# Kernel optimization log

Measured on AMD Instinct MI355X. Metric: run time of the kernel, lower is better.

Reference implementation:

```python
import jax, jax.numpy as jnp
import numpy as np

B, C, H, W = 8, 384, 32, 32
KEYS, HEADS, U = 16, 4, 1
VS = C // HEADS
N = H * W
BN_EPS = 1e-5


def setup_inputs() -> dict:
    key = jax.random.key(0)
    ks = jax.random.split(key, 8)
    x = jax.random.normal(ks[0], (B, C, H, W), dtype=jnp.float32)
    # 1x1 convs (spectral-normalized in torch; SN only rescales the weight,
    # so a plain weight matrix computes the same functional form)
    Wq = jax.random.normal(ks[1], (KEYS * HEADS, C), dtype=jnp.float32) * 0.02
    Wk = jax.random.normal(ks[2], (KEYS * U, C), dtype=jnp.float32) * 0.02
    Wv = jax.random.normal(ks[3], (VS * U, C), dtype=jnp.float32) * 0.02
    # BatchNorm affine params (torch code xavier-inits weight, zeros bias)
    gamma_q = jax.random.normal(ks[4], (KEYS * HEADS,), dtype=jnp.float32)
    beta_q = jnp.zeros((KEYS * HEADS,), dtype=jnp.float32)
    gamma_v = jax.random.normal(ks[5], (VS * U,), dtype=jnp.float32)
    beta_v = jnp.zeros((VS * U,), dtype=jnp.float32)
    pos_emb = jax.random.normal(ks[6], (N, N, KEYS, U), dtype=jnp.float32)
    return {"x": x, "Wq": Wq, "Wk": Wk, "Wv": Wv,
            "gamma_q": gamma_q, "beta_q": beta_q,
            "gamma_v": gamma_v, "beta_v": beta_v,
            "pos_emb": pos_emb}


def _bn(z, gamma, beta):
    # z: (B, Ch, N); BatchNorm2d in training mode: biased batch stats over (B, N)
    mean = jnp.mean(z, axis=(0, 2), keepdims=True)
    var = jnp.var(z, axis=(0, 2), keepdims=True)
    zn = (z - mean) * jax.lax.rsqrt(var + BN_EPS)
    return zn * gamma[None, :, None] + beta[None, :, None]


def reference(x, Wq, Wk, Wv, gamma_q, beta_q, gamma_v, beta_v, pos_emb):
    xf = x.reshape(B, C, N)                       # 1x1 conv == per-pixel matmul
    q = jnp.einsum('oc,bcn->bon', Wq, xf)         # (B, KEYS*HEADS, N)
    k = jnp.einsum('oc,bcn->bon', Wk, xf)         # (B, KEYS*U, N)
    v = jnp.einsum('oc,bcn->bon', Wv, xf)         # (B, VS*U, N)
    q = _bn(q, gamma_q, beta_q)
    v = _bn(v, gamma_v, beta_v)
    q = q.reshape(B, HEADS, KEYS, N)
    k = k.reshape(B, U, KEYS, N)
    v = v.reshape(B, U, VS, N)
    k = jax.nn.softmax(k, axis=-1)
    lambdac = jnp.einsum('bukm,buvm->bkv', k, v)          # content lambda
    Yc = jnp.einsum('bhkn,bkv->bhvn', q, lambdac)
    lambdap = jnp.einsum('nmku,buvm->bnkv', pos_emb, v)   # position lambda (B,N,K,V)
    Yp = jnp.einsum('bhkn,bnkv->bhvn', q, lambdap)
    Y = (Yc + Yp).reshape(B, C, H, W)
    return Y
```

## Files before the change

### kernel.cpp

```cpp
#include <hip/hip_runtime.h>

typedef __attribute__((ext_vector_type(8))) short short8;
typedef __attribute__((ext_vector_type(16))) float floatx16;
typedef __attribute__((ext_vector_type(4))) float floatx4;
typedef unsigned short ushort16_t;
typedef unsigned int uint32;

#define BB 8
#define CC 384
#define NPIX 1024
#define TOTCH 176
#define BN_EPS 1e-5f

__device__ __forceinline__ ushort16_t f2bf(float x) {
    uint32 u = __float_as_uint(x);
    u += 0x7FFFu + ((u >> 16) & 1u);
    return (ushort16_t)(u >> 16);
}
__device__ __forceinline__ uint32 pk2(float a, float b) {
    uint32 ua = __float_as_uint(a); ua += 0x7FFFu + ((ua >> 16) & 1u);
    uint32 ub = __float_as_uint(b); ub += 0x7FFFu + ((ub >> 16) & 1u);
    return (ua >> 16) | (ub & 0xFFFF0000u);
}
__device__ __forceinline__ void dma16(const ushort16_t* g, ushort16_t* l) {
    __builtin_amdgcn_global_load_lds(
        (const __attribute__((address_space(1))) uint32*)g,
        (__attribute__((address_space(3))) uint32*)l, 16, 0, 0);
}
__device__ __forceinline__ int div48(int x) {
    return (int)(((unsigned)x * 21846u) >> 20);
}


__global__ __launch_bounds__(256) void k_xt(const float* __restrict__ x,
    const float* __restrict__ Wq, const float* __restrict__ Wk,
    const float* __restrict__ Wv,
    ushort16_t* __restrict__ xbf, ushort16_t* __restrict__ wbf)
{
    int bx = blockIdx.x, t = threadIdx.x;
    if (bx < 256) {
        __shared__ __align__(16) ushort16_t T[32 * 392];
        int col0 = bx * 32;
        int b = col0 >> 10, nbase = col0 & 1023;
        const float* xb = x + (size_t)b * (CC * NPIX) + nbase;
        #pragma unroll
        for (int j = 0; j < 12; ++j) {
            int idx = t + 256 * j;
            int c = idx >> 3, ng = idx & 7;
            float4 f = *(const float4*)(xb + (size_t)c * NPIX + ng * 4);
            int n = ng * 4;
            T[(n + 0) * 392 + c] = f2bf(f.x);
            T[(n + 1) * 392 + c] = f2bf(f.y);
            T[(n + 2) * 392 + c] = f2bf(f.z);
            T[(n + 3) * 392 + c] = f2bf(f.w);
        }
        __syncthreads();
        #pragma unroll
        for (int j = 0; j < 6; ++j) {
            int task = t + 256 * j;
            int col = div48(task);
            int ch  = task - col * 48;
            uint4 w = *(const uint4*)&T[col * 392 + ch * 8];
            *(uint4*)&xbf[(size_t)(col0 + col) * CC + ch * 8] = w;
        }
    } else {
        #pragma unroll
        for (int jj = 0; jj < 9; ++jj) {
            int idx8 = ((bx - 256) * 9 + jj) * 256 + t;
            int row = div48(idx8);
            int g   = idx8 - row * 48;
            float4 f0, f1;
            if (row < 176) {
                const float* src;
                if (row < 64)       src = Wq + (size_t)row * CC;
                else if (row < 80)  src = Wk + (size_t)(row - 64) * CC;
                else                src = Wv + (size_t)(row - 80) * CC;
                f0 = *(const float4*)(src + g * 8);
                f1 = *(const float4*)(src + g * 8 + 4);
            } else {
                f0.x = f0.y = f0.z = f0.w = 0.f;
                f1 = f0;
            }
            uint4 w;
            w.x = pk2(f0.x, f0.y); w.y = pk2(f0.z, f0.w);
            w.z = pk2(f1.x, f1.y); w.w = pk2(f1.z, f1.w);
            *(uint4*)&wbf[(size_t)row * CC + g * 8] = w;
        }
    }
}

__global__ __launch_bounds__(256) void k_proj(const ushort16_t* __restrict__ xbf,
    const ushort16_t* __restrict__ wbf, float* __restrict__ qkv)
{
    int t = threadIdx.x;
    int wave = t >> 6, lane = t & 63;
    int ct = blockIdx.x * 4 + wave;
    int r0 = blockIdx.y * 16;
    int col = ct * 16 + (lane & 15);
    int kh  = lane >> 4;
    const ushort16_t* ap = wbf + (size_t)(r0 + (lane & 15)) * CC + kh * 8;
    const ushort16_t* bp = xbf + (size_t)col * CC + kh * 8;
    floatx4 acc = {0.f, 0.f, 0.f, 0.f};
    short8 a0 = *(const short8*)ap;
    short8 b0 = *(const short8*)bp;
    #pragma unroll
    for (int k = 1; k < 12; ++k) {
        short8 a1 = *(const short8*)(ap + k * 32);
        short8 b1 = *(const short8*)(bp + k * 32);
        acc = __builtin_amdgcn_mfma_f32_16x16x32_bf16(a0, b0, acc, 0, 0, 0);
        a0 = a1; b0 = b1;
    }
    acc = __builtin_amdgcn_mfma_f32_16x16x32_bf16(a0, b0, acc, 0, 0, 0);
    int b = col >> 10, n = col & 1023;
    #pragma unroll
    for (int r = 0; r < 4; ++r) {
        int ch = r0 + (lane >> 4) * 4 + r;
        qkv[((size_t)b * TOTCH + ch) * NPIX + n] = acc[r];
    }
}

__global__ __launch_bounds__(256) void k_bnsm(const float* __restrict__ qkv,
    const float* __restrict__ gq, const float* __restrict__ bq,
    const float* __restrict__ gv, const float* __restrict__ bv,
    float* __restrict__ sA, float* __restrict__ sB, float* __restrict__ ksm)
{
    int bx = blockIdx.x, tid = threadIdx.x;
    int wid = tid >> 6, lane = tid & 63;
    if (bx < 160) {
        int ch = bx;
        int row; float gamma, beta;
        if (ch < 64) { row = ch; gamma = gq[ch]; beta = bq[ch]; }
        else { int j = ch - 64; row = 80 + j; gamma = gv[j]; beta = bv[j]; }
        float s = 0.f, ss = 0.f;
        #pragma unroll
        for (int j = 0; j < 8; ++j) {
            int i4 = tid + 256 * j;
            int b = i4 >> 8, n4 = i4 & 255;
            float4 f = *(const float4*)(qkv + ((size_t)b * TOTCH + row) * NPIX
                                            + n4 * 4);
            s  += f.x + f.y + f.z + f.w;
            ss += f.x * f.x + f.y * f.y + f.z * f.z + f.w * f.w;
        }
        #pragma unroll
        for (int off = 32; off > 0; off >>= 1) {
            s  += __shfl_down(s, off);
            ss += __shfl_down(ss, off);
        }
        __shared__ float rs[4], rss[4];
        if (lane == 0) { rs[wid] = s; rss[wid] = ss; }
        __syncthreads();
        if (tid == 0) {
            float S  = rs[0] + rs[1] + rs[2] + rs[3];
            float SS = rss[0] + rss[1] + rss[2] + rss[3];
            float inv = 1.f / (BB * NPIX);
            float mean = S * inv;
            float var  = SS * inv - mean * mean;
            float a = gamma * rsqrtf(var + BN_EPS);
            sA[row] = a;
            sB[row] = beta - mean * a;
        }
    } else {
        int idx = bx - 160;
        int kc = idx & 15, b = idx >> 4;
        const float* rowp = qkv + ((size_t)b * TOTCH + 64 + kc) * NPIX;
        float4 v4 = *(const float4*)(rowp + tid * 4);
        float v[4] = {v4.x, v4.y, v4.z, v4.w};
        float mx = fmaxf(fmaxf(v[0], v[1]), fmaxf(v[2], v[3]));
        #pragma unroll
        for (int off = 32; off > 0; off >>= 1) mx = fmaxf(mx, __shfl_down(mx, off));
        __shared__ float sm[4], ssum[4];
        if (lane == 0) sm[wid] = mx;
        __syncthreads();
        mx = fmaxf(fmaxf(sm[0], sm[1]), fmaxf(sm[2], sm[3]));
        float e[4], s = 0.f;
        #pragma unroll
        for (int j = 0; j < 4; ++j) { e[j] = __expf(v[j] - mx); s += e[j]; }
        #pragma unroll
        for (int off = 32; off > 0; off >>= 1) s += __shfl_down(s, off);
        if (lane == 0) ssum[wid] = s;
        __syncthreads();
        float inv = 1.f / (ssum[0] + ssum[1] + ssum[2] + ssum[3]);
        float4 o;
        o.x = e[0] * inv; o.y = e[1] * inv; o.z = e[2] * inv; o.w = e[3] * inv;
        *(float4*)(ksm + ((size_t)b * 16 + kc) * NPIX + tid * 4) = o;
    }
}

__global__ __launch_bounds__(256) void k_packlc(const float* __restrict__ qkv,
    const float* __restrict__ sA, const float* __restrict__ sB,
    const float* __restrict__ ksm,
    ushort16_t* __restrict__ qt_g, ushort16_t* __restrict__ vt_g,
    ushort16_t* __restrict__ lc_g)
{
    int bx = blockIdx.x, t = threadIdx.x;
    if (bx < 128) {
        int bh = t & 31, nn = (t >> 5) & 7;
        int n = bx * 8 + nn;
        int b = bh >> 2, h = bh & 3;
        float vals[16];
        #pragma unroll
        for (int k = 0; k < 16; ++k) {
            int ch = h * 16 + k;
            vals[k] = qkv[((size_t)b * TOTCH + ch) * NPIX + n] * sA[ch] + sB[ch];
        }
        uint4 w0, w1;
        w0.x = pk2(vals[0], vals[1]);  w0.y = pk2(vals[2], vals[3]);
        w0.z = pk2(vals[4], vals[5]);  w0.w = pk2(vals[6], vals[7]);
        w1.x = pk2(vals[8], vals[9]);  w1.y = pk2(vals[10], vals[11]);
        w1.z = pk2(vals[12], vals[13]); w1.w = pk2(vals[14], vals[15]);
        *(uint4*)&qt_g[(size_t)n * 512 + bh * 8]       = w0;
        *(uint4*)&qt_g[(size_t)n * 512 + 256 + bh * 8] = w1;
    } else if (bx < 512) {
        int gi = (bx - 128) * 256 + t;
        int m8 = gi & 127;
        int vg = (gi >> 7) % 96;
        int b  = gi / (96 * 128);
        int m  = m8 * 8;
        int row = 80 + vg;
        float a = sA[row], bb = sB[row];
        const float* p = qkv + ((size_t)b * TOTCH + row) * NPIX + m;
        float4 f0 = *(const float4*)p;
        float4 f1 = *(const float4*)(p + 4);
        uint4 w;
        w.x = pk2(f0.x * a + bb, f0.y * a + bb);
        w.y = pk2(f0.z * a + bb, f0.w * a + bb);
        w.z = pk2(f1.x * a + bb, f1.y * a + bb);
        w.w = pk2(f1.z * a + bb, f1.w * a + bb);
        int mt = m >> 5, mq = (m >> 3) & 3;
        int vhh = vg / 48, vtt = (vg % 48) >> 4, vl = vg & 15;
        size_t idx = ((((size_t)b * 32 + mt) * 2 + vhh) * 3 + vtt) * 512
                   + mq * 128 + vl * 8;
        *(uint4*)&vt_g[idx] = w;
    } else {
        int gi = bx - 512;
        int v = gi % 96, b = gi / 96;
        int row = 80 + v;
        float a = sA[row], bb = sB[row];
        const float* vp = qkv + ((size_t)b * TOTCH + row) * NPIX;
        const float* kp = ksm + (size_t)b * 16 * NPIX;
        float acc[16];
        #pragma unroll
        for (int k = 0; k < 16; ++k) acc[k] = 0.f;
        for (int m = t; m < NPIX; m += 256) {
            float vv = vp[m] * a + bb;
            #pragma unroll
            for (int k = 0; k < 16; ++k) acc[k] += kp[k * NPIX + m] * vv;
        }
        #pragma unroll
        for (int k = 0; k < 16; ++k) {
            #pragma unroll
            for (int off = 32; off > 0; off >>= 1)
                acc[k] += __shfl_down(acc[k], off);
        }
        __shared__ float red[16][4];
        int wid = t >> 6, lane = t & 63;
        if (lane == 0) {
            #pragma unroll
            for (int k = 0; k < 16; ++k) red[k][wid] = acc[k];
        }
        __syncthreads();
        int vhh = v / 48, vtt = (v % 48) >> 4, vl = v & 15;
        size_t plane = ((size_t)(b * 2 + vhh) * 3 + vtt) * 512;
        if (t < 16) {
            int k = t;
            float val = red[k][0] + red[k][1] + red[k][2] + red[k][3];
            lc_g[plane + (k >> 3) * 128 + vl * 8 + (k & 7)] = f2bf(val);
        } else if (t < 18) {
            int mq = 2 + (t - 16);
            uint4 z; z.x = z.y = z.z = z.w = 0u;
            *(uint4*)&lc_g[plane + mq * 128 + vl * 8] = z;
        }
    }
}

__global__ __launch_bounds__(512, 2) void k_main(const float* __restrict__ pos,
    const ushort16_t* __restrict__ qt_g, const ushort16_t* __restrict__ vt_g,
    const ushort16_t* __restrict__ lc_g, float* __restrict__ out)
{
    __shared__ __align__(16) ushort16_t V_s[2][12288];
    __shared__ __align__(16) ushort16_t S_s[2][8192];
    int tid  = threadIdx.x;
    int lane = tid & 63;
    int wave = tid >> 6;
    int n0 = blockIdx.x * 8;
    int vh = blockIdx.y;

    int col1 = lane & 31, half = lane >> 5;
    int pb = col1 >> 2, ph = col1 & 3;
    int pplane = pb * 2 + (ph >> 1);
    int pf = pplane & 7;
    int pcb = ph & 1;
    int b2 = wave;

    short8 qfr = *(const short8*)(qt_g + (size_t)(n0 + wave) * 512
                                  + half * 256 + col1 * 8);

    floatx4 acc[2][3];
    #pragma unroll
    for (int hg = 0; hg < 2; ++hg)
        #pragma unroll
        for (int vt = 0; vt < 3; ++vt)
            acc[hg][vt] = floatx4{0.f, 0.f, 0.f, 0.f};

    floatx16 z16;
    #pragma unroll
    for (int i = 0; i < 16; ++i) z16[i] = 0.f;

    const float* pA = pos + ((size_t)(n0 + wave) * 1024 + col1) * 16 + half * 8;

    float4 a0 = *(const float4*)pA;
    float4 a1 = *(const float4*)(pA + 4);
    {
        const ushort16_t* src = vt_g + (size_t)((b2 * 32 * 2 + vh) * 3) * 512;
        #pragma unroll
        for (int j = 0; j < 3; ++j)
            dma16(src + j * 512 + lane * 8, &V_s[0][b2 * 1536 + j * 512]);
    }

    for (int it = 0; it < 32; ++it) {
        float4 na0, na1;
        if (it < 31) {
            const float* p = pA + (size_t)(it + 1) * 512;
            na0 = *(const float4*)p;
            na1 = *(const float4*)(p + 4);
        }
        {
            uint4 aw;
            aw.x = pk2(a0.x, a0.y); aw.y = pk2(a0.z, a0.w);
            aw.z = pk2(a1.x, a1.y); aw.w = pk2(a1.z, a1.w);
            short8 afr = *(short8*)&aw;
            floatx16 d = __builtin_amdgcn_mfma_f32_32x32x16_bf16(
                afr, qfr, z16, 0, 0, 0);
            int nx = wave ^ pf;
            ushort16_t* Sb = S_s[it & 1];
            #pragma unroll
            for (int q = 0; q < 4; ++q) {
                int c = q * 16 + pcb * 8 + nx;
                uint2 wv;
                wv.x = pk2(d[q * 4 + 0], d[q * 4 + 1]);
                wv.y = pk2(d[q * 4 + 2], d[q * 4 + 3]);
                *(uint2*)&Sb[pplane * 512 + c * 8 + half * 4] = wv;
            }
        }
        __syncthreads();
        if (it < 31) {
            const ushort16_t* src = vt_g
                + (size_t)(((b2 * 32 + it + 1) * 2 + vh) * 3) * 512;
            #pragma unroll
            for (int j = 0; j < 3; ++j)
                dma16(src + j * 512 + lane * 8,
                      &V_s[(it + 1) & 1][b2 * 1536 + j * 512]);
        }
        {
            const ushort16_t* Vb = V_s[it & 1];
            const ushort16_t* Sb = S_s[it & 1];
            short8 av[3];
            #pragma unroll
            for (int vt = 0; vt < 3; ++vt)
                av[vt] = *(const short8*)&Vb[b2 * 1536 + vt * 512 + lane * 8];
            #pragma unroll
            for (int hg = 0; hg < 2; ++hg) {
                int p2 = b2 * 2 + hg, f2 = p2 & 7;
                short8 bs = *(const short8*)&Sb[p2 * 512
                    + ((lane >> 4) * 16 + ((lane & 15) ^ f2)) * 8];
                #pragma unroll
                for (int vt = 0; vt < 3; ++vt)
                    acc[hg][vt] = __builtin_amdgcn_mfma_f32_16x16x32_bf16(
                        av[vt], bs, acc[hg][vt], 0, 0, 0);
            }
        }
        a0 = na0; a1 = na1;
    }

    {
        const ushort16_t* src = lc_g + (size_t)((b2 * 2 + vh) * 3) * 512;
        #pragma unroll
        for (int j = 0; j < 3; ++j)
            dma16(src + j * 512 + lane * 8, &V_s[0][b2 * 1536 + j * 512]);
    }
    {
        int c = half * 16 + pcb * 8 + (wave ^ pf);
        *(short8*)&S_s[0][pplane * 512 + c * 8] = qfr;
        int zp = tid >> 5, zr = tid & 31;
        int zc = (2 + (zr >> 4)) * 16 + ((zr & 15) ^ (zp & 7));
        uint4 z; z.x = z.y = z.z = z.w = 0u;
        *(uint4*)&S_s[0][zp * 512 + zc * 8] = z;
    }
    __syncthreads();
    {
        short8 av[3];
        #pragma unroll
        for (int vt = 0; vt < 3; ++vt)
            av[vt] = *(const short8*)&V_s[0][b2 * 1536 + vt * 512 + lane * 8];
        #pragma unroll
        for (int hg = 0; hg < 2; ++hg) {
            int p2 = b2 * 2 + hg, f2 = p2 & 7;
            short8 bs = *(const short8*)&S_s[0][p2 * 512
                + ((lane >> 4) * 16 + ((lane & 15) ^ f2)) * 8];
            #pragma unroll
            for (int vt = 0; vt < 3; ++vt)
                acc[hg][vt] = __builtin_amdgcn_mfma_f32_16x16x32_bf16(
                    av[vt], bs, acc[hg][vt], 0, 0, 0);
        }
    }

    {
        int cn = lane & 15;
        int nloc = cn & 7;
        #pragma unroll
        for (int hg = 0; hg < 2; ++hg) {
            int h = hg * 2 + (cn >> 3);
            #pragma unroll
            for (int vt = 0; vt < 3; ++vt) {
                #pragma unroll
                for (int r = 0; r < 4; ++r) {
                    int v = vh * 48 + vt * 16 + (lane >> 4) * 4 + r;
                    out[(size_t)(b2 * 384 + h * 96 + v) * 1024 + n0 + nloc]
                        = acc[hg][vt][r];
                }
            }
        }
    }
}

extern "C" void kernel_launch(void* const* d_in, const int* in_sizes, int n_in,
                              void* d_out, int out_size, void* d_ws, size_t ws_size,
                              hipStream_t stream) {
    const float* x   = (const float*)d_in[0];
    const float* Wq  = (const float*)d_in[1];
    const float* Wk  = (const float*)d_in[2];
    const float* Wv  = (const float*)d_in[3];
    const float* gq  = (const float*)d_in[4];
    const float* bq  = (const float*)d_in[5];
    const float* gv  = (const float*)d_in[6];
    const float* bv  = (const float*)d_in[7];
    const float* pos = (const float*)d_in[8];
    float* out = (float*)d_out;
    float* ws  = (float*)d_ws;

    float* qkv = ws;
    float* sA  = ws + 1441792;
    float* sB  = ws + 1441968;
    float* ksm = ws + 1442144;
    ushort16_t* qt_g = (ushort16_t*)(ws + 1573216);
    ushort16_t* vt_g = (ushort16_t*)(ws + 1835360);
    ushort16_t* lc_g = (ushort16_t*)(ws + 2228576);
    ushort16_t* xbf  = (ushort16_t*)(ws + 2240864);
    ushort16_t* wbf  = (ushort16_t*)(ws + 3813728);

    k_xt<<<dim3(260), dim3(256), 0, stream>>>(x, Wq, Wk, Wv, xbf, wbf);
    k_proj<<<dim3(128, 11), dim3(256), 0, stream>>>(xbf, wbf, qkv);
    k_bnsm<<<dim3(288), dim3(256), 0, stream>>>(qkv, gq, bq, gv, bv, sA, sB, ksm);
    k_packlc<<<dim3(1280), dim3(256), 0, stream>>>(qkv, sA, sB, ksm,
                                                   qt_g, vt_g, lc_g);
    k_main<<<dim3(128, 2), dim3(512), 0, stream>>>(pos, qt_g, vt_g, lc_g, out);
}
```

Measured before the change: 184.5 us.

## Split main kernel over m-chunks with atomic accumulation and direct V register loads

The main kernel gains a third grid dimension that splits the 32-step m loop into 4 chunks of 8, so four times as many blocks run. Partial results are combined with atomic adds into an output that is zeroed by a memset first. V tiles are now loaded straight into registers instead of through async LDS DMA, and the content-lambda term is added only by chunk 0. The packlc lambda-content reduction is also vectorised with float4 loads. The cost is extra atomic traffic, the memset, and redundant q fragment loads per chunk, in exchange for more parallelism across the GPU.

```diff
diff --git a/kernel.cpp b/kernel.cpp
--- a/kernel.cpp
+++ b/kernel.cpp
@@ -21,11 +21,6 @@
     uint32 ua = __float_as_uint(a); ua += 0x7FFFu + ((ua >> 16) & 1u);
     uint32 ub = __float_as_uint(b); ub += 0x7FFFu + ((ub >> 16) & 1u);
     return (ua >> 16) | (ub & 0xFFFF0000u);
-}
-__device__ __forceinline__ void dma16(const ushort16_t* g, ushort16_t* l) {
-    __builtin_amdgcn_global_load_lds(
-        (const __attribute__((address_space(1))) uint32*)g,
-        (__attribute__((address_space(3))) uint32*)l, 16, 0, 0);
 }
 __device__ __forceinline__ int div48(int x) {
     return (int)(((unsigned)x * 21846u) >> 20);
@@ -238,13 +233,16 @@
         float a = sA[row], bb = sB[row];
         const float* vp = qkv + ((size_t)b * TOTCH + row) * NPIX;
         const float* kp = ksm + (size_t)b * 16 * NPIX;
+        float4 vv = *(const float4*)(vp + t * 4);
+        float4 vhat;
+        vhat.x = vv.x * a + bb; vhat.y = vv.y * a + bb;
+        vhat.z = vv.z * a + bb; vhat.w = vv.w * a + bb;
         float acc[16];
         #pragma unroll
-        for (int k = 0; k < 16; ++k) acc[k] = 0.f;
-        for (int m = t; m < NPIX; m += 256) {
-            float vv = vp[m] * a + bb;
-            #pragma unroll
-            for (int k = 0; k < 16; ++k) acc[k] += kp[k * NPIX + m] * vv;
+        for (int k = 0; k < 16; ++k) {
+            float4 kk = *(const float4*)(kp + (size_t)k * NPIX + t * 4);
+            acc[k] = kk.x * vhat.x + kk.y * vhat.y
+                   + kk.z * vhat.z + kk.w * vhat.w;
         }
         #pragma unroll
         for (int k = 0; k < 16; ++k) {
@@ -277,13 +275,13 @@
     const ushort16_t* __restrict__ qt_g, const ushort16_t* __restrict__ vt_g,
     const ushort16_t* __restrict__ lc_g, float* __restrict__ out)
 {
-    __shared__ __align__(16) ushort16_t V_s[2][12288];
     __shared__ __align__(16) ushort16_t S_s[2][8192];
     int tid  = threadIdx.x;
     int lane = tid & 63;
     int wave = tid >> 6;
     int n0 = blockIdx.x * 8;
     int vh = blockIdx.y;
+    int ms = blockIdx.z;
 
     int col1 = lane & 31, half = lane >> 5;
     int pb = col1 >> 2, ph = col1 & 3;
@@ -307,22 +305,28 @@
     for (int i = 0; i < 16; ++i) z16[i] = 0.f;
 
     const float* pA = pos + ((size_t)(n0 + wave) * 1024 + col1) * 16 + half * 8;
-
-    float4 a0 = *(const float4*)pA;
-    float4 a1 = *(const float4*)(pA + 4);
-    {
-        const ushort16_t* src = vt_g + (size_t)((b2 * 32 * 2 + vh) * 3) * 512;
-        #pragma unroll
-        for (int j = 0; j < 3; ++j)
-            dma16(src + j * 512 + lane * 8, &V_s[0][b2 * 1536 + j * 512]);
-    }
-
-    for (int it = 0; it < 32; ++it) {
+    const ushort16_t* pV = vt_g + (size_t)b2 * 98304 + (size_t)vh * 1536
+                         + lane * 8;
+
+    int it0 = ms * 8;
+    float4 a0 = *(const float4*)(pA + (size_t)it0 * 512);
+    float4 a1 = *(const float4*)(pA + (size_t)it0 * 512 + 4);
+    const ushort16_t* v0p = pV + (size_t)it0 * 3072;
+    short8 av0 = *(const short8*)(v0p);
+    short8 av1 = *(const short8*)(v0p + 512);
+    short8 av2 = *(const short8*)(v0p + 1024);
+
+    for (int i = 0; i < 8; ++i) {
         float4 na0, na1;
-        if (it < 31) {
-            const float* p = pA + (size_t)(it + 1) * 512;
+        short8 nv0, nv1, nv2;
+        if (i < 7) {
+            const float* p = pA + (size_t)(it0 + i + 1) * 512;
             na0 = *(const float4*)p;
             na1 = *(const float4*)(p + 4);
+            const ushort16_t* vp = pV + (size_t)(it0 + i + 1) * 3072;
+            nv0 = *(const short8*)(vp);
+            nv1 = *(const short8*)(vp + 512);
+            nv2 = *(const short8*)(vp + 1024);
         }
         {
             uint4 aw;
@@ -332,7 +336,7 @@
             floatx16 d = __builtin_amdgcn_mfma_f32_32x32x16_bf16(
                 afr, qfr, z16, 0, 0, 0);
             int nx = wave ^ pf;
-            ushort16_t* Sb = S_s[it & 1];
+            ushort16_t* Sb = S_s[i & 1];
             #pragma unroll
             for (int q = 0; q < 4; ++q) {
                 int c = q * 16 + pcb * 8 + nx;
@@ -343,64 +347,49 @@
             }
         }
         __syncthreads();
-        if (it < 31) {
-            const ushort16_t* src = vt_g
-                + (size_t)(((b2 * 32 + it + 1) * 2 + vh) * 3) * 512;
-            #pragma unroll
-            for (int j = 0; j < 3; ++j)
-                dma16(src + j * 512 + lane * 8,
-                      &V_s[(it + 1) & 1][b2 * 1536 + j * 512]);
-        }
         {
-            const ushort16_t* Vb = V_s[it & 1];
-            const ushort16_t* Sb = S_s[it & 1];
-            short8 av[3];
-            #pragma unroll
-            for (int vt = 0; vt < 3; ++vt)
-                av[vt] = *(const short8*)&Vb[b2 * 1536 + vt * 512 + lane * 8];
+            const ushort16_t* Sb = S_s[i & 1];
             #pragma unroll
             for (int hg = 0; hg < 2; ++hg) {
                 int p2 = b2 * 2 + hg, f2 = p2 & 7;
                 short8 bs = *(const short8*)&Sb[p2 * 512
                     + ((lane >> 4) * 16 + ((lane & 15) ^ f2)) * 8];
-                #pragma unroll
-                for (int vt = 0; vt < 3; ++vt)
-                    acc[hg][vt] = __builtin_amdgcn_mfma_f32_16x16x32_bf16(
-                        av[vt], bs, acc[hg][vt], 0, 0, 0);
+                acc[hg][0] = __builtin_amdgcn_mfma_f32_16x16x32_bf16(
+                    av0, bs, acc[hg][0], 0, 0, 0);
+                acc[hg][1] = __builtin_amdgcn_mfma_f32_16x16x32_bf16(
+                    av1, bs, acc[hg][1], 0, 0, 0);
+                acc[hg][2] = __builtin_amdgcn_mfma_f32_16x16x32_bf16(
+                    av2, bs, acc[hg][2], 0, 0, 0);
             }
         }
-        a0 = na0; a1 = na1;
-    }
-
-    {
-        const ushort16_t* src = lc_g + (size_t)((b2 * 2 + vh) * 3) * 512;
-        #pragma unroll
-        for (int j = 0; j < 3; ++j)
-            dma16(src + j * 512 + lane * 8, &V_s[0][b2 * 1536 + j * 512]);
-    }
-    {
-        int c = half * 16 + pcb * 8 + (wave ^ pf);
-        *(short8*)&S_s[0][pplane * 512 + c * 8] = qfr;
-        int zp = tid >> 5, zr = tid & 31;
-        int zc = (2 + (zr >> 4)) * 16 + ((zr & 15) ^ (zp & 7));
-        uint4 z; z.x = z.y = z.z = z.w = 0u;
-        *(uint4*)&S_s[0][zp * 512 + zc * 8] = z;
-    }
-    __syncthreads();
-    {
-        short8 av[3];
-        #pragma unroll
-        for (int vt = 0; vt < 3; ++vt)
-            av[vt] = *(const short8*)&V_s[0][b2 * 1536 + vt * 512 + lane * 8];
+        if (i < 7) { a0 = na0; a1 = na1; av0 = nv0; av1 = nv1; av2 = nv2; }
+    }
+
+    if (ms == 0) {
+        const ushort16_t* lsrc = lc_g + (size_t)(b2 * 2 + vh) * 1536 + lane * 8;
+        short8 lv0 = *(const short8*)(lsrc);
+        short8 lv1 = *(const short8*)(lsrc + 512);
+        short8 lv2 = *(const short8*)(lsrc + 1024);
+        {
+            int c = half * 16 + pcb * 8 + (wave ^ pf);
+            *(short8*)&S_s[0][pplane * 512 + c * 8] = qfr;
+            int zp = tid >> 5, zr = tid & 31;
+            int zc = (2 + (zr >> 4)) * 16 + ((zr & 15) ^ (zp & 7));
+            uint4 z; z.x = z.y = z.z = z.w = 0u;
+            *(uint4*)&S_s[0][zp * 512 + zc * 8] = z;
+        }
+        __syncthreads();
         #pragma unroll
         for (int hg = 0; hg < 2; ++hg) {
             int p2 = b2 * 2 + hg, f2 = p2 & 7;
             short8 bs = *(const short8*)&S_s[0][p2 * 512
                 + ((lane >> 4) * 16 + ((lane & 15) ^ f2)) * 8];
-            #pragma unroll
-            for (int vt = 0; vt < 3; ++vt)
-                acc[hg][vt] = __builtin_amdgcn_mfma_f32_16x16x32_bf16(
-                    av[vt], bs, acc[hg][vt], 0, 0, 0);
+            acc[hg][0] = __builtin_amdgcn_mfma_f32_16x16x32_bf16(
+                lv0, bs, acc[hg][0], 0, 0, 0);
+            acc[hg][1] = __builtin_amdgcn_mfma_f32_16x16x32_bf16(
+                lv1, bs, acc[hg][1], 0, 0, 0);
+            acc[hg][2] = __builtin_amdgcn_mfma_f32_16x16x32_bf16(
+                lv2, bs, acc[hg][2], 0, 0, 0);
         }
     }
 
@@ -415,8 +404,9 @@
                 #pragma unroll
                 for (int r = 0; r < 4; ++r) {
                     int v = vh * 48 + vt * 16 + (lane >> 4) * 4 + r;
-                    out[(size_t)(b2 * 384 + h * 96 + v) * 1024 + n0 + nloc]
-                        = acc[hg][vt][r];
+                    unsafeAtomicAdd(
+                        &out[(size_t)(b2 * 384 + h * 96 + v) * 1024 + n0 + nloc],
+                        acc[hg][vt][r]);
                 }
             }
         }
@@ -448,10 +438,11 @@
     ushort16_t* xbf  = (ushort16_t*)(ws + 2240864);
     ushort16_t* wbf  = (ushort16_t*)(ws + 3813728);
 
+    hipMemsetAsync(d_out, 0, (size_t)out_size * sizeof(float), stream);
     k_xt<<<dim3(260), dim3(256), 0, stream>>>(x, Wq, Wk, Wv, xbf, wbf);
     k_proj<<<dim3(128, 11), dim3(256), 0, stream>>>(xbf, wbf, qkv);
     k_bnsm<<<dim3(288), dim3(256), 0, stream>>>(qkv, gq, bq, gv, bv, sA, sB, ksm);
     k_packlc<<<dim3(1280), dim3(256), 0, stream>>>(qkv, sA, sB, ksm,
                                                    qt_g, vt_g, lc_g);
-    k_main<<<dim3(128, 2), dim3(512), 0, stream>>>(pos, qt_g, vt_g, lc_g, out);
-}
+    k_main<<<dim3(128, 2, 4), dim3(512), 0, stream>>>(pos, qt_g, vt_g, lc_g, out);
+}
```

Measured after the change: 232.2 us. 1.26x slower.
